# Kernel optimization log

Measured on AMD Instinct MI355X. Metric: run time of the kernel, lower is better.

## Reference

```python
import jax, jax.numpy as jnp
import numpy as np

HIDDEN_N = 6
B, C, H, W = 16, 4, 512, 512


def _make_filters():
    identity = jnp.array([[0., 0., 0.], [0., 1., 0.], [0., 0., 0.]], jnp.float32)
    sobel_x = jnp.array([[-1., 0., 1.], [-2., 0., 2.], [-1., 0., 1.]], jnp.float32)
    lap = jnp.array([[1., 2., 1.], [2., -12., 2.], [1., 2., 1.]], jnp.float32)
    # [4, 3, 3]: identity, sobel_x, sobel_y (= sobel_x.T), laplacian
    return jnp.stack([identity, sobel_x, sobel_x.T, lap])


def setup_inputs() -> dict:
    key = jax.random.key(0)
    ks = jax.random.split(key, 6)
    x = jax.random.normal(ks[0], (B, C, H, W), jnp.float32)
    filters = _make_filters()
    # Conv2d(16, hidden_n, 1): weight [hidden_n, 16], kaiming-uniform-like init
    s1 = 1.0 / np.sqrt(16.0)
    w1_w = jax.random.uniform(ks[1], (HIDDEN_N, 16), jnp.float32, -s1, s1)
    w1_b = jax.random.uniform(ks[2], (HIDDEN_N,), jnp.float32, -s1, s1)
    s2 = 1.0 / np.sqrt(float(HIDDEN_N))
    # zero_w2=True: w2 weight zeroed at init (bias kept random)
    w2_w = jnp.zeros((4, HIDDEN_N), jnp.float32)
    w2_b = jax.random.uniform(ks[3], (4,), jnp.float32, -s2, s2)
    w3_w = jax.random.uniform(ks[4], (4, HIDDEN_N), jnp.float32, -s2, s2)
    w3_b = jax.random.uniform(ks[5], (4,), jnp.float32, -s2, s2)
    return {"x": x, "filters": filters, "w1_w": w1_w, "w1_b": w1_b,
            "w2_w": w2_w, "w2_b": w2_b, "w3_w": w3_w, "w3_b": w3_b}


def _perchannel_conv(x, filters):
    # x: [B, C, H, W], filters: [4, 3, 3] -> [B, C*4, H, W] (channel-major, filter-minor)
    b, c, h, w = x.shape
    xp = jnp.pad(x, ((0, 0), (0, 0), (1, 1), (1, 1)), mode="wrap")  # circular pad
    lhs = xp.reshape(b * c, 1, h + 2, w + 2)
    y = jax.lax.conv_general_dilated(
        lhs, filters[:, None], window_strides=(1, 1), padding="VALID",
        dimension_numbers=("NCHW", "OIHW", "NCHW"))  # [b*c, 4, h, w]
    return y.reshape(b, c * 4, h, w)


def _conv1x1(h, w, b):
    # 1x1 conv == channel contraction
    return jnp.einsum("bchw,oc->bohw", h, w) + b[None, :, None, None]


def reference(x, filters, w1_w, w1_b, w2_w, w2_b, w3_w, w3_b):
    y = _perchannel_conv(x, filters)                     # [B, 16, H, W]
    hid = jax.nn.relu(_conv1x1(y, w1_w, w1_b))           # [B, 6, H, W]
    y_upd = jnp.tanh(_conv1x1(hid, w2_w, w2_b))          # [B, 4, H, W]
    gate = jax.nn.sigmoid(_conv1x1(hid, w3_w, w3_b))     # [B, 4, H, W]
    return x * gate + (1.0 - gate) * y_upd
```

## Files before the change

### kernel.cpp

```cpp
#include <hip/hip_runtime.h>


constexpr int Bn = 16, Cn = 4, Hn = 512, Wn = 512, HID = 6;

__device__ __forceinline__ float frcp(float v) { return __builtin_amdgcn_rcpf(v); }

__global__ __launch_bounds__(256) void nca_fused8(
    const float* __restrict__ x,
    const float* __restrict__ w1w, const float* __restrict__ w1b,
    const float* __restrict__ w2w, const float* __restrict__ w2b,
    const float* __restrict__ w3w, const float* __restrict__ w3b,
    float* __restrict__ out)
{
    const int G = Wn / 8;
    int tid = blockIdx.x * 256 + threadIdx.x;
    int g = tid & (G - 1);
    int h = (tid >> 6) & (Hn - 1);
    int b = tid >> 15;

    int w0 = g << 3;
    int hm = (h == 0)      ? Hn - 1 : h - 1;
    int hp = (h == Hn - 1) ? 0      : h + 1;
    int wl = (w0 == 0)       ? Wn - 1 : w0 - 1;
    int wr = (w0 + 8 == Wn)  ? 0      : w0 + 8;

    const size_t plane = (size_t)Hn * Wn;
    const float* xb = x + (size_t)b * Cn * plane;

    float acc[HID][8];
    #pragma unroll
    for (int o = 0; o < HID; ++o) {
        float bv = w1b[o];
        #pragma unroll
        for (int i = 0; i < 8; ++i) acc[o][i] = bv;
    }

    float xc[Cn][8];

    #pragma unroll
    for (int c = 0; c < Cn; ++c) {
        const float* xp = xb + c * plane;
        const float* rt = xp + (size_t)hm * Wn;
        const float* rm = xp + (size_t)h  * Wn;
        const float* rb = xp + (size_t)hp * Wn;
        float4 ta = *(const float4*)(rt + w0), tb = *(const float4*)(rt + w0 + 4);
        float4 ma = *(const float4*)(rm + w0), mb = *(const float4*)(rm + w0 + 4);
        float4 ba = *(const float4*)(rb + w0), bb = *(const float4*)(rb + w0 + 4);
        float t[10] = { rt[wl], ta.x, ta.y, ta.z, ta.w, tb.x, tb.y, tb.z, tb.w, rt[wr] };
        float m[10] = { rm[wl], ma.x, ma.y, ma.z, ma.w, mb.x, mb.y, mb.z, mb.w, rm[wr] };
        float q[10] = { rb[wl], ba.x, ba.y, ba.z, ba.w, bb.x, bb.y, bb.z, bb.w, rb[wr] };

        float s[10], dd[10];
        #pragma unroll
        for (int j = 0; j < 10; ++j) {
            s[j]  = fmaf(2.f, m[j], t[j] + q[j]);
            dd[j] = q[j] - t[j];
        }

        #pragma unroll
        for (int i = 0; i < 8; ++i) {
            int j = i + 1;
            float mc = m[j];
            float y1 = s[j + 1] - s[j - 1];
            float y2 = fmaf(2.f, dd[j], dd[j - 1] + dd[j + 1]);
            float y3 = fmaf(-16.f, mc,
                       fmaf(2.f, s[j], s[j - 1] + s[j + 1]));
            xc[c][i] = mc;
            #pragma unroll
            for (int o = 0; o < HID; ++o) {
                acc[o][i] = fmaf(w1w[o*16 + c*4 + 0], mc,
                            fmaf(w1w[o*16 + c*4 + 1], y1,
                            fmaf(w1w[o*16 + c*4 + 2], y2,
                            fmaf(w1w[o*16 + c*4 + 3], y3, acc[o][i]))));
            }
        }
    }

    #pragma unroll
    for (int o = 0; o < HID; ++o)
        #pragma unroll
        for (int i = 0; i < 8; ++i)
            acc[o][i] = fmaxf(acc[o][i], 0.f);

    float* ob = out + (size_t)b * Cn * plane + (size_t)h * Wn + w0;
    #pragma unroll
    for (int j = 0; j < Cn; ++j) {
        float res[8];
        #pragma unroll
        for (int i = 0; i < 8; ++i) {
            float u = w2b[j], gg = w3b[j];
            #pragma unroll
            for (int o = 0; o < HID; ++o) {
                u  = fmaf(w2w[j*HID + o], acc[o][i], u);
                gg = fmaf(w3w[j*HID + o], acc[o][i], gg);
            }
            float th = 1.f - 2.f * frcp(__expf(2.f * u) + 1.f);
            float sg = frcp(1.f + __expf(-gg));
            res[i] = fmaf(sg, xc[j][i] - th, th);
        }
        *(float4*)(ob + j * plane)     = make_float4(res[0], res[1], res[2], res[3]);
        *(float4*)(ob + j * plane + 4) = make_float4(res[4], res[5], res[6], res[7]);
    }
}

extern "C" void kernel_launch(void* const* d_in, const int* in_sizes, int n_in,
                              void* d_out, int out_size, void* d_ws, size_t ws_size,
                              hipStream_t stream) {
    const float* x   = (const float*)d_in[0];
    const float* w1w = (const float*)d_in[2];
    const float* w1b = (const float*)d_in[3];
    const float* w2w = (const float*)d_in[4];
    const float* w2b = (const float*)d_in[5];
    const float* w3w = (const float*)d_in[6];
    const float* w3b = (const float*)d_in[7];
    float* out = (float*)d_out;

    int total  = Bn * Hn * (Wn / 8);
    int blocks = total / 256;
    nca_fused8<<<blocks, 256, 0, stream>>>(x, w1w, w1b, w2w, w2b, w3w, w3b, out);
}
```

Before: 148.9 us.

## Process vertical strips of rows per thread with rolling row registers

Result: slower. 184.8 us (+24.1%).

```diff
diff --git a/kernel.cpp b/kernel.cpp
--- a/kernel.cpp
+++ b/kernel.cpp
@@ -1,105 +1,123 @@
 #include <hip/hip_runtime.h>
 
 
-constexpr int Bn = 16, Cn = 4, Hn = 512, Wn = 512, HID = 6;
+constexpr int Bn = 16, Cn = 4, Hn = 512, Wn = 512, HID = 6, R = 4;
 
 __device__ __forceinline__ float frcp(float v) { return __builtin_amdgcn_rcpf(v); }
 
-__global__ __launch_bounds__(256) void nca_fused8(
+__global__ __launch_bounds__(256) void nca_strip(
     const float* __restrict__ x,
     const float* __restrict__ w1w, const float* __restrict__ w1b,
     const float* __restrict__ w2w, const float* __restrict__ w2b,
     const float* __restrict__ w3w, const float* __restrict__ w3b,
     float* __restrict__ out)
 {
-    const int G = Wn / 8;
+    const int S = Hn / R;
     int tid = blockIdx.x * 256 + threadIdx.x;
-    int g = tid & (G - 1);
-    int h = (tid >> 6) & (Hn - 1);
-    int b = tid >> 15;
+    int g = tid & 127;
+    int s = (tid >> 7) & (S - 1);
+    int b = tid >> 14;
 
-    int w0 = g << 3;
-    int hm = (h == 0)      ? Hn - 1 : h - 1;
-    int hp = (h == Hn - 1) ? 0      : h + 1;
-    int wl = (w0 == 0)       ? Wn - 1 : w0 - 1;
-    int wr = (w0 + 8 == Wn)  ? 0      : w0 + 8;
+    int w0 = g << 2;
+    int wl = (w0 == 0)      ? Wn - 1 : w0 - 1;
+    int wr = (w0 + 4 == Wn) ? 0      : w0 + 4;
+    int h0 = s * R;
+    int hm = (h0 == 0) ? Hn - 1 : h0 - 1;
 
     const size_t plane = (size_t)Hn * Wn;
     const float* xb = x + (size_t)b * Cn * plane;
 
-    float acc[HID][8];
-    #pragma unroll
-    for (int o = 0; o < HID; ++o) {
-        float bv = w1b[o];
-        #pragma unroll
-        for (int i = 0; i < 8; ++i) acc[o][i] = bv;
-    }
-
-    float xc[Cn][8];
-
+    float t[Cn][6], m[Cn][6];
     #pragma unroll
     for (int c = 0; c < Cn; ++c) {
         const float* xp = xb + c * plane;
         const float* rt = xp + (size_t)hm * Wn;
-        const float* rm = xp + (size_t)h  * Wn;
-        const float* rb = xp + (size_t)hp * Wn;
-        float4 ta = *(const float4*)(rt + w0), tb = *(const float4*)(rt + w0 + 4);
-        float4 ma = *(const float4*)(rm + w0), mb = *(const float4*)(rm + w0 + 4);
-        float4 ba = *(const float4*)(rb + w0), bb = *(const float4*)(rb + w0 + 4);
-        float t[10] = { rt[wl], ta.x, ta.y, ta.z, ta.w, tb.x, tb.y, tb.z, tb.w, rt[wr] };
-        float m[10] = { rm[wl], ma.x, ma.y, ma.z, ma.w, mb.x, mb.y, mb.z, mb.w, rm[wr] };
-        float q[10] = { rb[wl], ba.x, ba.y, ba.z, ba.w, bb.x, bb.y, bb.z, bb.w, rb[wr] };
+        const float* rm = xp + (size_t)h0 * Wn;
+        float4 t4 = *(const float4*)(rt + w0);
+        float4 m4 = *(const float4*)(rm + w0);
+        t[c][0] = rt[wl]; t[c][1] = t4.x; t[c][2] = t4.y; t[c][3] = t4.z; t[c][4] = t4.w; t[c][5] = rt[wr];
+        m[c][0] = rm[wl]; m[c][1] = m4.x; m[c][2] = m4.y; m[c][3] = m4.z; m[c][4] = m4.w; m[c][5] = rm[wr];
+    }
 
-        float s[10], dd[10];
+    #pragma unroll
+    for (int r = 0; r < R; ++r) {
+        int h  = h0 + r;
+        int hb = (h + 1) & (Hn - 1);
+
+        float bot[Cn][6];
         #pragma unroll
-        for (int j = 0; j < 10; ++j) {
-            s[j]  = fmaf(2.f, m[j], t[j] + q[j]);
-            dd[j] = q[j] - t[j];
+        for (int c = 0; c < Cn; ++c) {
+            const float* rp = xb + c * plane + (size_t)hb * Wn;
+            float4 b4 = *(const float4*)(rp + w0);
+            bot[c][0] = rp[wl]; bot[c][1] = b4.x; bot[c][2] = b4.y; bot[c][3] = b4.z; bot[c][4] = b4.w; bot[c][5] = rp[wr];
+        }
+
+        float acc[HID][4];
+        #pragma unroll
+        for (int o = 0; o < HID; ++o) {
+            float bv = w1b[o];
+            #pragma unroll
+            for (int i = 0; i < 4; ++i) acc[o][i] = bv;
         }
 
         #pragma unroll
-        for (int i = 0; i < 8; ++i) {
-            int j = i + 1;
-            float mc = m[j];
-            float y1 = s[j + 1] - s[j - 1];
-            float y2 = fmaf(2.f, dd[j], dd[j - 1] + dd[j + 1]);
-            float y3 = fmaf(-16.f, mc,
-                       fmaf(2.f, s[j], s[j - 1] + s[j + 1]));
-            xc[c][i] = mc;
+        for (int c = 0; c < Cn; ++c) {
+            float sc[6], dc[6];
             #pragma unroll
-            for (int o = 0; o < HID; ++o) {
-                acc[o][i] = fmaf(w1w[o*16 + c*4 + 0], mc,
-                            fmaf(w1w[o*16 + c*4 + 1], y1,
-                            fmaf(w1w[o*16 + c*4 + 2], y2,
-                            fmaf(w1w[o*16 + c*4 + 3], y3, acc[o][i]))));
+            for (int j = 0; j < 6; ++j) {
+                sc[j] = fmaf(2.f, m[c][j], t[c][j] + bot[c][j]);
+                dc[j] = bot[c][j] - t[c][j];
+            }
+            #pragma unroll
+            for (int i = 0; i < 4; ++i) {
+                int j = i + 1;
+                float mc = m[c][j];
+                float y1 = sc[j + 1] - sc[j - 1];
+                float y2 = fmaf(2.f, dc[j], dc[j - 1] + dc[j + 1]);
+                float y3 = fmaf(-16.f, mc,
+                           fmaf(2.f, sc[j], sc[j - 1] + sc[j + 1]));
+                #pragma unroll
+                for (int o = 0; o < HID; ++o) {
+                    acc[o][i] = fmaf(w1w[o*16 + c*4 + 0], mc,
+                                fmaf(w1w[o*16 + c*4 + 1], y1,
+                                fmaf(w1w[o*16 + c*4 + 2], y2,
+                                fmaf(w1w[o*16 + c*4 + 3], y3, acc[o][i]))));
+                }
             }
         }
-    }
 
-    #pragma unroll
-    for (int o = 0; o < HID; ++o)
         #pragma unroll
-        for (int i = 0; i < 8; ++i)
-            acc[o][i] = fmaxf(acc[o][i], 0.f);
+        for (int o = 0; o < HID; ++o)
+            #pragma unroll
+            for (int i = 0; i < 4; ++i)
+                acc[o][i] = fmaxf(acc[o][i], 0.f);
 
-    float* ob = out + (size_t)b * Cn * plane + (size_t)h * Wn + w0;
-    #pragma unroll
-    for (int j = 0; j < Cn; ++j) {
-        float res[8];
+        float* ob = out + (size_t)b * Cn * plane + (size_t)h * Wn + w0;
         #pragma unroll
-        for (int i = 0; i < 8; ++i) {
-            float u = w2b[j], gg = w3b[j];
+        for (int j = 0; j < Cn; ++j) {
+            float res[4];
             #pragma unroll
-            for (int o = 0; o < HID; ++o) {
-                u  = fmaf(w2w[j*HID + o], acc[o][i], u);
-                gg = fmaf(w3w[j*HID + o], acc[o][i], gg);
+            for (int i = 0; i < 4; ++i) {
+                float u = w2b[j], gg = w3b[j];
+                #pragma unroll
+                for (int o = 0; o < HID; ++o) {
+                    u  = fmaf(w2w[j*HID + o], acc[o][i], u);
+                    gg = fmaf(w3w[j*HID + o], acc[o][i], gg);
+                }
+                float th = 1.f - 2.f * frcp(__expf(2.f * u) + 1.f);
+                float sg = frcp(1.f + __expf(-gg));
+                res[i] = fmaf(sg, m[j][i + 1] - th, th);
             }
-            float th = 1.f - 2.f * frcp(__expf(2.f * u) + 1.f);
-            float sg = frcp(1.f + __expf(-gg));
-            res[i] = fmaf(sg, xc[j][i] - th, th);
+            *(float4*)(ob + (size_t)j * plane) = make_float4(res[0], res[1], res[2], res[3]);
         }
-        *(float4*)(ob + j * plane)     = make_float4(res[0], res[1], res[2], res[3]);
-        *(float4*)(ob + j * plane + 4) = make_float4(res[4], res[5], res[6], res[7]);
+
+        #pragma unroll
+        for (int c = 0; c < Cn; ++c)
+            #pragma unroll
+            for (int k = 0; k < 6; ++k) {
+                t[c][k] = m[c][k];
+                m[c][k] = bot[c][k];
+            }
     }
 }
 
@@ -115,7 +133,7 @@
     const float* w3b = (const float*)d_in[7];
     float* out = (float*)d_out;
 
-    int total  = Bn * Hn * (Wn / 8);
+    int total  = Bn * (Hn / R) * (Wn / 4);
     int blocks = total / 256;
-    nca_fused8<<<blocks, 256, 0, stream>>>(x, w1w, w1b, w2w, w2b, w3w, w3b, out);
+    nca_strip<<<blocks, 256, 0, stream>>>(x, w1w, w1b, w2w, w2b, w3w, w3b, out);
 }
```
